# Performance work log

Measured on AMD Instinct MI355X. Metric: run time of the kernel, lower is better.

Reference implementation:

```python
import jax, jax.numpy as jnp
import numpy as np

N_LEVELS = 4
F_DIM = 2
B = 1_000_000
SIZES = [12 * ((2 ** (l - 1)) ** 2 + 2) for l in range(1, N_LEVELS + 1)]  # [36, 72, 216, 792]
MAX_SIZE = max(SIZES)  # 792
NPIX = [12 * (2 ** i) ** 2 for i in range(N_LEVELS)]  # [12, 48, 192, 768]


def setup_inputs() -> dict:
    key = jax.random.key(0)
    ks = jax.random.split(key, 6)
    # learned table, init uniform(-1e-4, 1e-4) as in the torch module
    params = jax.random.uniform(ks[0], (N_LEVELS, MAX_SIZE, F_DIM),
                                minval=-1e-4, maxval=1e-4, dtype=jnp.float32)
    # per-level HEALPix pixel indices, each in [0, npix_level)
    pixel_index = jnp.stack([
        jax.random.randint(jax.random.fold_in(ks[1], i), (B,), 0, NPIX[i], dtype=jnp.int32)
        for i in range(N_LEVELS)])
    neigh = jnp.stack([
        jax.random.randint(jax.random.fold_in(ks[2], i), (8, B), 0, NPIX[i], dtype=jnp.int32)
        for i in range(N_LEVELS)])
    drop = jax.random.uniform(ks[3], (N_LEVELS, 8, B)) < 0.05
    neigh_index = jnp.where(drop, jnp.int32(-1), neigh)
    # latlon in radians: theta in [0, pi], phi in [0, 2*pi)
    u_p = jax.random.uniform(ks[4], (N_LEVELS, B, 2))
    pixel_latlon = jnp.stack([u_p[..., 0] * jnp.pi, u_p[..., 1] * (2 * jnp.pi)], axis=-1).astype(jnp.float32)
    u_n = jax.random.uniform(ks[5], (N_LEVELS, 8 * B, 2))
    neigh_latlon = jnp.stack([u_n[..., 0] * jnp.pi, u_n[..., 1] * (2 * jnp.pi)], axis=-1).astype(jnp.float32)
    return {"params": params, "pixel_latlon": pixel_latlon, "neigh_latlon": neigh_latlon,
            "pixel_index": pixel_index, "neigh_index": neigh_index}


def reference(params, pixel_latlon, neigh_latlon, pixel_index, neigh_index):
    L, _, F = params.shape  # [L, max_size, F]
    Bp = pixel_index.shape[1]
    # index_preprocessing: -1 -> max(index)+1, build keep-mask
    nflat = neigh_index.reshape(L, -1)  # [L, 8B]
    miss = nflat == -1
    nflat = jnp.where(miss, nflat.max() + 1, nflat)
    nmask = (~miss).astype(params.dtype)  # [L, 8B]
    pidx = jnp.where(pixel_index == -1, pixel_index.max() + 1, pixel_index)  # [L, B]
    # gathers from the parameter table
    neigh_reps = jnp.take_along_axis(params, nflat[..., None], axis=1)   # [L, 8B, F]
    my_reps = jnp.take_along_axis(params, pidx[..., None], axis=1)       # [L, B, F]
    # inverse-distance weights (equirectangular "great circle" per source)
    my_ll = jnp.broadcast_to(pixel_latlon[:, None], (L, 8, Bp, 2)).reshape(L, 8 * Bp, 2)
    d = jnp.sqrt((neigh_latlon[..., 1] - my_ll[..., 1]) ** 2 +
                 (neigh_latlon[..., 0] - my_ll[..., 0]) ** 2)  # [L, 8B]
    d = jnp.where(jnp.isinf(d), d.min(), d)
    w = 1.0 / d
    # weight, mask, sum over 8 neighbors, add residual
    out = (neigh_reps * w[..., None]).reshape(L, 8, Bp, F) * nmask.reshape(L, 8, Bp)[..., None]
    out = out.sum(axis=1) + my_reps  # [L, B, F]
    # faithful to torch: reshape(4, -1).t().reshape(-1, L*F)
    out = out.reshape(4, -1).T.reshape(-1, L * F)
    return out.astype(jnp.float32)
```

## Files before the change

### kernel.cpp

```cpp
#include <hip/hip_runtime.h>


#define NLEV 4
#define MAXSZ 792
#define TABSZ (NLEV * MAXSZ * 2)
#define PPB 128
#define OSTRIDE 12

__global__ __launch_bounds__(512) void heal_encoding_kernel(
    const float* __restrict__ params,
    const float* __restrict__ pixel_latlon,
    const float* __restrict__ neigh_latlon,
    const int*   __restrict__ pixel_index,
    const int*   __restrict__ neigh_index,
    float* __restrict__ out,
    int B)
{
    __shared__ float stab[TABSZ];
    __shared__ float sout[PPB * OSTRIDE];

    const int tid = threadIdx.x;
    const int bl  = tid & (PPB - 1);
    const int l   = tid >> 7;
    const int b_raw = blockIdx.x * PPB + bl;
    const int b = min(b_raw, B - 1);

    const float2* pll2 = (const float2*)pixel_latlon;
    const float2* nll2 = (const float2*)neigh_latlon;

    int   pi  = pixel_index[l * B + b];
    float2 pll = pll2[l * B + b];
    int    ni[8];
    float2 nl[8];
    #pragma unroll
    for (int j = 0; j < 8; ++j) {
        ni[j] = neigh_index[(l * 8 + j) * B + b];
        nl[j] = nll2[(l * 8 + j) * B + b];
    }

    {
        const float4* p4  = (const float4*)params;
        float4*       st4 = (float4*)stab;
        for (int i = tid; i < TABSZ / 4; i += 512)
            st4[i] = p4[i];
    }
    __syncthreads();

    const float2* sp2 = (const float2*)stab;
    const int lbase = l * MAXSZ;

    float a0 = 0.0f, a1 = 0.0f;
    #pragma unroll
    for (int j = 0; j < 8; ++j) {
        float dth = nl[j].x - pll.x;
        float dph = nl[j].y - pll.y;
        float d   = sqrtf(dth * dth + dph * dph);
        float w   = (ni[j] >= 0) ? (1.0f / d) : 0.0f;
        float2 r  = sp2[lbase + (ni[j] >= 0 ? ni[j] : 0)];
        a0 += w * r.x;
        a1 += w * r.y;
    }
    float2 m = sp2[lbase + (pi < 0 ? 768 : pi)];
    a0 += m.x;
    a1 += m.y;

    sout[bl * OSTRIDE + l]     = a0;
    sout[bl * OSTRIDE + 4 + l] = a1;
    __syncthreads();

    if (tid < 2 * PPB) {
        int px = tid >> 1;
        int h  = tid & 1;
        int bo = blockIdx.x * PPB + px;
        if (bo < B) {
            float4 v = *(const float4*)&sout[px * OSTRIDE + 4 * h];
            ((float4*)(out + (size_t)bo * 8))[h] = v;
        }
    }
}

extern "C" void kernel_launch(void* const* d_in, const int* in_sizes, int n_in,
                              void* d_out, int out_size, void* d_ws, size_t ws_size,
                              hipStream_t stream) {
    const float* params       = (const float*)d_in[0];
    const float* pixel_latlon = (const float*)d_in[1];
    const float* neigh_latlon = (const float*)d_in[2];
    const int*   pixel_index  = (const int*)d_in[3];
    const int*   neigh_index  = (const int*)d_in[4];
    float* out = (float*)d_out;

    int B = in_sizes[3] / NLEV;
    int blocks = (B + PPB - 1) / PPB;
    heal_encoding_kernel<<<blocks, 512, 0, stream>>>(
        params, pixel_latlon, neigh_latlon, pixel_index, neigh_index, out, B);
}
```

Measured before the change: 459.6 us.

## Use persistent grid-stride waves with wave-shuffle output transpose

Replaces the one-block-per-128-pixels launch with a persistent grid capped at 2048 blocks of 256 threads. Each 64-lane wave handles 16 pixels across the 4 levels and loops over pixel groups, so the 25 KB parameter table is copied into LDS once per block instead of once per 128 pixels. The output transpose now uses wave shuffles instead of LDS staging and a second barrier. The cost is that each wave reads only 16 contiguous elements per input row, which makes global loads less coalesced.

```diff
diff --git a/kernel.cpp b/kernel.cpp
--- a/kernel.cpp
+++ b/kernel.cpp
@@ -4,10 +4,8 @@
 #define NLEV 4
 #define MAXSZ 792
 #define TABSZ (NLEV * MAXSZ * 2)
-#define PPB 128
-#define OSTRIDE 12
 
-__global__ __launch_bounds__(512) void heal_encoding_kernel(
+__global__ __launch_bounds__(256, 4) void heal_encoding_kernel(
     const float* __restrict__ params,
     const float* __restrict__ pixel_latlon,
     const float* __restrict__ neigh_latlon,
@@ -17,64 +15,76 @@
     int B)
 {
     __shared__ float stab[TABSZ];
-    __shared__ float sout[PPB * OSTRIDE];
+    {
+        const float4* p4 = (const float4*)params;
+        float4*       s4 = (float4*)stab;
+        for (int i = threadIdx.x; i < TABSZ / 4; i += 256)
+            s4[i] = p4[i];
+    }
+    __syncthreads();
+    const float2* sp2 = (const float2*)stab;
 
-    const int tid = threadIdx.x;
-    const int bl  = tid & (PPB - 1);
-    const int l   = tid >> 7;
-    const int b_raw = blockIdx.x * PPB + bl;
-    const int b = min(b_raw, B - 1);
+    const int lane = threadIdx.x & 63;
+    const int l    = lane >> 4;
+    const int p    = lane & 15;
+    const int lbase = l * MAXSZ;
+
+    const int  l0 = (2 * (lane & 3)) & 3;
+    const bool f1 = (lane & 3) >= 2;
+    const int  sA = (lane >> 2) + 16 * l0;
+    const int  sB = sA + 16;
 
     const float2* pll2 = (const float2*)pixel_latlon;
     const float2* nll2 = (const float2*)neigh_latlon;
 
-    int   pi  = pixel_index[l * B + b];
-    float2 pll = pll2[l * B + b];
-    int    ni[8];
-    float2 nl[8];
-    #pragma unroll
-    for (int j = 0; j < 8; ++j) {
-        ni[j] = neigh_index[(l * 8 + j) * B + b];
-        nl[j] = nll2[(l * 8 + j) * B + b];
-    }
+    const int wavesPerBlock = 256 / 64;
+    const int w = blockIdx.x * wavesPerBlock + (threadIdx.x >> 6);
+    const int totalWaves = gridDim.x * wavesPerBlock;
+    const int nGroups = (B + 15) >> 4;
 
-    {
-        const float4* p4  = (const float4*)params;
-        float4*       st4 = (float4*)stab;
-        for (int i = tid; i < TABSZ / 4; i += 512)
-            st4[i] = p4[i];
-    }
-    __syncthreads();
+    for (int g = w; g < nGroups; g += totalWaves) {
+        const int px  = g * 16 + p;
+        const int pxc = min(px, B - 1);
 
-    const float2* sp2 = (const float2*)stab;
-    const int lbase = l * MAXSZ;
+        int    pi  = pixel_index[l * B + pxc];
+        float2 pll = pll2[l * B + pxc];
+        int    ni[8];
+        float2 nl[8];
+        #pragma unroll
+        for (int j = 0; j < 8; ++j) {
+            const int off = (l * 8 + j) * B + pxc;
+            ni[j] = neigh_index[off];
+            nl[j] = nll2[off];
+        }
 
-    float a0 = 0.0f, a1 = 0.0f;
-    #pragma unroll
-    for (int j = 0; j < 8; ++j) {
-        float dth = nl[j].x - pll.x;
-        float dph = nl[j].y - pll.y;
-        float d   = sqrtf(dth * dth + dph * dph);
-        float w   = (ni[j] >= 0) ? (1.0f / d) : 0.0f;
-        float2 r  = sp2[lbase + (ni[j] >= 0 ? ni[j] : 0)];
-        a0 += w * r.x;
-        a1 += w * r.y;
-    }
-    float2 m = sp2[lbase + (pi < 0 ? 768 : pi)];
-    a0 += m.x;
-    a1 += m.y;
+        float a0 = 0.0f, a1 = 0.0f;
+        #pragma unroll
+        for (int j = 0; j < 8; ++j) {
+            float dth = nl[j].x - pll.x;
+            float dph = nl[j].y - pll.y;
+            float d   = sqrtf(dth * dth + dph * dph);
+            float wgt = (ni[j] >= 0) ? (1.0f / d) : 0.0f;
+            float2 r  = sp2[lbase + (ni[j] >= 0 ? ni[j] : 0)];
+            a0 += wgt * r.x;
+            a1 += wgt * r.y;
+        }
+        float2 m = sp2[lbase + (pi < 0 ? 768 : pi)];
+        a0 += m.x;
+        a1 += m.y;
 
-    sout[bl * OSTRIDE + l]     = a0;
-    sout[bl * OSTRIDE + 4 + l] = a1;
-    __syncthreads();
+        float r0 = __shfl(a0, sA, 64);
+        float r1 = __shfl(a1, sA, 64);
+        float r2 = __shfl(a0, sB, 64);
+        float r3 = __shfl(a1, sB, 64);
+        float lo = f1 ? r1 : r0;
+        float hi = f1 ? r3 : r2;
 
-    if (tid < 2 * PPB) {
-        int px = tid >> 1;
-        int h  = tid & 1;
-        int bo = blockIdx.x * PPB + px;
-        if (bo < B) {
-            float4 v = *(const float4*)&sout[px * OSTRIDE + 4 * h];
-            ((float4*)(out + (size_t)bo * 8))[h] = v;
+        const size_t obase = (size_t)g * 128 + 2 * lane;
+        if (g * 16 + 16 <= B) {
+            *(float2*)(out + obase) = make_float2(lo, hi);
+        } else {
+            if (obase     < (size_t)B * 8) out[obase]     = lo;
+            if (obase + 1 < (size_t)B * 8) out[obase + 1] = hi;
         }
     }
 }
@@ -90,7 +100,10 @@
     float* out = (float*)d_out;
 
     int B = in_sizes[3] / NLEV;
-    int blocks = (B + PPB - 1) / PPB;
-    heal_encoding_kernel<<<blocks, 512, 0, stream>>>(
+    int nGroups = (B + 15) / 16;
+    int blocks = (nGroups + 3) / 4;
+    if (blocks > 2048) blocks = 2048;
+    if (blocks < 1) blocks = 1;
+    heal_encoding_kernel<<<blocks, 256, 0, stream>>>(
         params, pixel_latlon, neigh_latlon, pixel_index, neigh_index, out, B);
 }
```

After: 467.8 us. Within noise of the previous version (+1.8%).
